# Performance work log

Measured on AMD Instinct MI355X. Metric: run time of the kernel, lower is better.

## Reference

```python
import jax, jax.numpy as jnp
import numpy as np

K, D = 2048, 256
B, H, W = 16, 64, 64
DECAY = 0.99
EPS = 1e-05


def setup_inputs() -> dict:
    key = jax.random.key(0)
    k1, k2, k3 = jax.random.split(key, 3)
    z_e = jax.random.normal(k1, (B, D, H, W), dtype=jnp.float32)
    codebook = jax.random.normal(k2, (K, D), dtype=jnp.float32)
    ema_count = jnp.zeros((K,), dtype=jnp.float32)
    ema_weight = jax.random.normal(k3, (K, D), dtype=jnp.float32)
    return {"z_e": z_e, "codebook": codebook, "ema_count": ema_count, "ema_weight": ema_weight}


def reference(z_e, codebook, ema_count, ema_weight):
    b, d, h, w = z_e.shape
    k = codebook.shape[0]
    # [B, D, H, W] -> [B*H*W, D]
    flat = jnp.transpose(z_e, (0, 2, 3, 1)).reshape(-1, d)
    # squared euclidean distances to each code: [N, K]
    dist = (jnp.sum(flat * flat, axis=1, keepdims=True)
            - 2.0 * (flat @ codebook.T)
            + jnp.sum(codebook * codebook, axis=1))
    idx = jnp.argmin(dist, axis=1)  # [N] int
    # gather nearest codes -> [B, D, H, W]
    z_q = jnp.transpose(codebook[idx].reshape(b, h, w, d), (0, 3, 1, 2))
    # EMA statistics (training path, no_grad in torch)
    n = jax.ops.segment_sum(jnp.ones_like(idx, dtype=flat.dtype), idx, num_segments=k)  # [K]
    dw = jax.ops.segment_sum(flat, idx, num_segments=k)  # [K, D]
    new_ema_count = ema_count * DECAY + (1.0 - DECAY) * n
    new_ema_weight = ema_weight * DECAY + (1.0 - DECAY) * dw
    new_codebook = new_ema_weight / (new_ema_count + EPS)[:, None]
    # commitment loss and straight-through estimator
    loss_commit = jnp.mean(jnp.square(z_e - z_q))
    z_q_st = z_e + jax.lax.stop_gradient(z_q - z_e)
    return (z_q_st, idx.reshape(b, h, w), loss_commit,
            new_codebook, new_ema_count, new_ema_weight)
```

## Files before the change

kernel.cpp:

```cpp
#include <hip/hip_runtime.h>
#include <hip/hip_bf16.h>


#define KC 2048
#define DD 256
#define NB 16
#define HWS 4096
#define NPTS 65536
#define DECAYF 0.99f
#define ONEMD 0.01f
#define EPSF 1e-5f
#define NCH 2
#define MARGIN 0.0625f
#define CHPTS 32
#define FPT 64
#define NLOSS 4096

typedef __attribute__((ext_vector_type(8))) short short8v;
typedef __attribute__((ext_vector_type(16))) float f32x16;

#define WS_IDX     0
#define WS_SORTED  262144
#define WS_CNTI    524288
#define WS_START   532480
#define WS_CURSOR  540672
#define WS_FLAGCNT 548864
#define WS_FLAGS   549120
#define WS_LOSSP   549120
#define WS_CNORM   811264
#define WS_PART    819456
#define WS_CBH     5013760
#define WS_CBL     6062336
#define WS_ZH      7110912
#define WS_ZL      40665344
#define WS_NEED_MFMA 74219776ULL
#define WS_NEED_MID  5013760ULL

#define OUT_ZQ   0
#define OUT_IDX  16777216
#define OUT_LOSS (OUT_IDX + NPTS)
#define OUT_CB   (OUT_LOSS + 1)
#define OUT_CNT  (OUT_CB + KC*DD)
#define OUT_W    (OUT_CNT + KC)

static __device__ __forceinline__ unsigned short f2bf_rn(float x) {
    unsigned u = __builtin_bit_cast(unsigned, x);
    unsigned r = (u + 0x7FFFu + ((u >> 16) & 1u)) >> 16;
    return (unsigned short)r;
}
static __device__ __forceinline__ float bf2f(unsigned short h) {
    unsigned u = ((unsigned)h) << 16;
    return __builtin_bit_cast(float, u);
}
static __device__ __forceinline__ void gload_lds16(const unsigned short* g,
                                                   unsigned short* l) {
    __builtin_amdgcn_global_load_lds(
        (const __attribute__((address_space(1))) void*)g,
        (__attribute__((address_space(3))) void*)l, 16, 0, 0);
}

__global__ __launch_bounds__(256) void prep_kernel(const float* __restrict__ z_e,
                                                   const float* __restrict__ cb,
                                                   float* __restrict__ cnorm,
                                                   unsigned short* __restrict__ cbs_h,
                                                   unsigned short* __restrict__ cbs_l,
                                                   unsigned short* __restrict__ zh,
                                                   unsigned short* __restrict__ zl,
                                                   int* __restrict__ cnti,
                                                   int* __restrict__ flagcnt) {
    const int tid = threadIdx.x;
    if (blockIdx.x >= 4096) {
        int k = (blockIdx.x - 4096) * 256 + tid;
        cnti[k] = 0;
        if (k == 0) *flagcnt = 0;
        const int ct = k >> 5, lc = k & 31;
        const float4* row = reinterpret_cast<const float4*>(cb + (size_t)k * DD);
        float s = 0.f;
        #pragma unroll 4
        for (int chunk = 0; chunk < 32; ++chunk) {
            float4 v0 = row[chunk * 2], v1 = row[chunk * 2 + 1];
            float v[8] = {v0.x, v0.y, v0.z, v0.w, v1.x, v1.y, v1.z, v1.w};
            unsigned short hh[8], ll[8];
            #pragma unroll
            for (int j = 0; j < 8; ++j) {
                s += v[j] * v[j];
                hh[j] = f2bf_rn(v[j]);
                ll[j] = f2bf_rn(v[j] - bf2f(hh[j]));
            }
            const int ks = chunk >> 1, h = chunk & 1;
            size_t dst = (size_t)ct * 8192 + ks * 512 + (h * 32 + lc) * 8;
            *reinterpret_cast<ushort4*>(cbs_h + dst)     = *(ushort4*)&hh[0];
            *reinterpret_cast<ushort4*>(cbs_h + dst + 4) = *(ushort4*)&hh[4];
            *reinterpret_cast<ushort4*>(cbs_l + dst)     = *(ushort4*)&ll[0];
            *reinterpret_cast<ushort4*>(cbs_l + dst + 4) = *(ushort4*)&ll[4];
        }
        cnorm[k] = s;
        return;
    }
    __shared__ float t_lds[64][65];
    const int bid = blockIdx.x;
    const int hw0 = (bid & 63) * 64;
    const int d0 = ((bid >> 6) & 3) * 64;
    const int b = bid >> 8;
    const float* src = z_e + (size_t)b * DD * HWS;
    #pragma unroll
    for (int i = 0; i < 16; ++i) {
        int li = tid + i * 256;
        int d = li >> 6, hw = li & 63;
        t_lds[d][hw] = src[(size_t)(d0 + d) * HWS + hw0 + hw];
    }
    __syncthreads();
    #pragma unroll
    for (int i = 0; i < 16; ++i) {
        int li = tid + i * 256;
        int p = li >> 6, d = li & 63;
        float x = t_lds[d][p];
        unsigned short h = f2bf_rn(x);
        unsigned short l = f2bf_rn(x - bf2f(h));
        size_t o = ((size_t)b * HWS + hw0 + p) * DD + d0 + d;
        zh[o] = h; zl[o] = l;
    }
}

__global__ __launch_bounds__(256) void cnorm_kernel(const float* __restrict__ cb,
                                                    float* __restrict__ cnorm) {
    int k = blockIdx.x * 256 + threadIdx.x;
    if (k < KC) {
        const float4* row = reinterpret_cast<const float4*>(cb + (size_t)k * DD);
        float s = 0.f;
        #pragma unroll 8
        for (int i = 0; i < DD / 4; ++i) {
            float4 v = row[i];
            s += v.x * v.x + v.y * v.y + v.z * v.z + v.w * v.w;
        }
        cnorm[k] = s;
    }
}

__global__ __launch_bounds__(256, 2) void argmin_mfma_kernel(const unsigned short* __restrict__ zh,
                                                             const unsigned short* __restrict__ zl,
                                                             const unsigned short* __restrict__ cbs_h,
                                                             const unsigned short* __restrict__ cbs_l,
                                                             const float* __restrict__ cnorm,
                                                             int* __restrict__ idx_out,
                                                             int* __restrict__ cnti,
                                                             int* __restrict__ flagcnt,
                                                             int* __restrict__ flaglist,
                                                             unsigned long long* __restrict__ fixmin) {
    __shared__ unsigned short lds_cb[2][2][16][512];

    const int tid = threadIdx.x;
    const int w = tid >> 6, lane = tid & 63;
    const int lc = lane & 31, h = lane >> 5;
    const int p = blockIdx.x * 128 + w * 32 + lc;

    const short8v* zhp = reinterpret_cast<const short8v*>(zh + (size_t)p * DD + h * 8);
    const short8v* zlp = reinterpret_cast<const short8v*>(zl + (size_t)p * DD + h * 8);
    short8v bh[16], bl[16];
    #pragma unroll
    for (int ks = 0; ks < 16; ++ks) { bh[ks] = zhp[ks * 2]; bl[ks] = zlp[ks * 2]; }

    auto stage = [&](int ct, int buf) {
        #pragma unroll
        for (int j = 0; j < 8; ++j) {
            const int inst = w * 8 + j;
            const int part = inst >> 4;
            const int ks = inst & 15;
            const unsigned short* src =
                (part ? cbs_l : cbs_h) + (size_t)ct * 8192 + ks * 512 + lane * 8;
            gload_lds16(src, &lds_cb[buf][part][ks][0]);
        }
    };

    float bv1 = 3.4e38f, bv2 = 3.4e38f;
    int bi1 = 0;
    int cur = 0;

    stage(0, 0);
    __syncthreads();

    for (int ct = 0; ct < KC / 32; ++ct) {
        if (ct + 1 < KC / 32) stage(ct + 1, cur ^ 1);

        f32x16 a0, a1, a2;
        #pragma unroll
        for (int i = 0; i < 16; ++i) { a0[i] = 0.f; a1[i] = 0.f; a2[i] = 0.f; }
        #pragma unroll
        for (int ks = 0; ks < 16; ++ks) {
            short8v ah = *reinterpret_cast<const short8v*>(&lds_cb[cur][0][ks][lane * 8]);
            short8v al = *reinterpret_cast<const short8v*>(&lds_cb[cur][1][ks][lane * 8]);
            a0 = __builtin_amdgcn_mfma_f32_32x32x16_bf16(ah, bh[ks], a0, 0, 0, 0);
            a1 = __builtin_amdgcn_mfma_f32_32x32x16_bf16(ah, bl[ks], a1, 0, 0, 0);
            a2 = __builtin_amdgcn_mfma_f32_32x32x16_bf16(al, bh[ks], a2, 0, 0, 0);
        }
        const float* cnb = cnorm + ct * 32 + h * 4;
        #pragma unroll
        for (int g = 0; g < 4; ++g) {
            float4 cn = *reinterpret_cast<const float4*>(cnb + g * 8);
            float cna[4] = {cn.x, cn.y, cn.z, cn.w};
            #pragma unroll
            for (int q = 0; q < 4; ++q) {
                float dot = a0[g * 4 + q] + a1[g * 4 + q] + a2[g * 4 + q];
                float v = fmaf(dot, -2.0f, cna[q]);
                int k = ct * 32 + g * 8 + h * 4 + q;
                bool lt = v < bv1;
                bv2 = fminf(bv2, fmaxf(v, bv1));
                bv1 = fminf(bv1, v);
                bi1 = lt ? k : bi1;
            }
        }
        __syncthreads();
        cur ^= 1;
    }

    float ov1 = __shfl_xor(bv1, 32, 64);
    float ov2 = __shfl_xor(bv2, 32, 64);
    int   oi1 = __shfl_xor(bi1, 32, 64);
    float nv1 = fminf(bv1, ov1);
    float nv2 = fminf(fmaxf(bv1, ov1), fminf(bv2, ov2));
    int ni1 = (ov1 < bv1 || (ov1 == bv1 && oi1 < bi1)) ? oi1 : bi1;

    if (h == 0) {
        idx_out[p] = ni1;
        atomicAdd(&cnti[ni1], 1);
        if (nv2 - nv1 < MARGIN) {
            int pos = atomicAdd(flagcnt, 1);
            flaglist[pos] = p;
            fixmin[pos] = ~0ULL;
        }
    }
}

__global__ __launch_bounds__(256) void fixup_part_kernel(const float* __restrict__ z_e,
                                                         const float* __restrict__ cb,
                                                         const float* __restrict__ cnorm,
                                                         const int* __restrict__ flagcnt,
                                                         const int* __restrict__ flaglist,
                                                         unsigned long long* __restrict__ fixmin) {
    __shared__ float As[64][FPT + 4];
    __shared__ float Bs[64][64 + 4];
    __shared__ float rv[FPT][16];
    __shared__ int   ri[FPT][16];
    __shared__ int   zo[FPT];

    const int tid = threadIdx.x;
    const int tx = tid & 15, ty = tid >> 4;
    const int tot = *flagcnt;
    const int base = blockIdx.x * FPT;
    if (base >= tot) return;
    const int cnt = min(FPT, tot - base);
    const int kt = blockIdx.y * 64;

    if (tid < FPT) {
        int n = flaglist[base + ((tid < cnt) ? tid : 0)];
        zo[tid] = (n >> 12) * DD * HWS + (n & 4095);
    }
    __syncthreads();

    float acc[4][4] = {};
    for (int dc = 0; dc < DD; dc += 64) {
        #pragma unroll
        for (int i = 0; i < 16; ++i) {
            int li = tid + i * 256;
            int d = li >> 6, pp = li & 63;
            As[d][pp] = z_e[(size_t)zo[pp] + (size_t)(dc + d) * HWS];
        }
        #pragma unroll
        for (int i = 0; i < 16; ++i) {
            int li = tid + i * 256;
            int k = li >> 6, d = li & 63;
            Bs[d][k] = cb[(size_t)(kt + k) * DD + dc + d];
        }
        __syncthreads();
        #pragma unroll
        for (int d = 0; d < 64; ++d) {
            const float4 a4 = *reinterpret_cast<const float4*>(&As[d][ty * 4]);
            const float4 b4 = *reinterpret_cast<const float4*>(&Bs[d][tx * 4]);
            const float a[4] = {a4.x, a4.y, a4.z, a4.w};
            const float bb[4] = {b4.x, b4.y, b4.z, b4.w};
            #pragma unroll
            for (int j = 0; j < 4; ++j)
                #pragma unroll
                for (int i = 0; i < 4; ++i)
                    acc[j][i] = fmaf(a[j], bb[i], acc[j][i]);
        }
        __syncthreads();
    }

    float bestv[4]; int besti[4];
    #pragma unroll
    for (int j = 0; j < 4; ++j) { bestv[j] = 3.4e38f; besti[j] = 0; }
    #pragma unroll
    for (int i = 0; i < 4; ++i) {
        int k = kt + tx * 4 + i;
        float c = cnorm[k];
        #pragma unroll
        for (int j = 0; j < 4; ++j) {
            float dist = c - 2.0f * acc[j][i];
            if (dist < bestv[j]) { bestv[j] = dist; besti[j] = k; }
        }
    }
    #pragma unroll
    for (int j = 0; j < 4; ++j) { rv[ty * 4 + j][tx] = bestv[j]; ri[ty * 4 + j][tx] = besti[j]; }
    __syncthreads();

    if (tid < cnt) {
        float bv = rv[tid][0]; int bi = ri[tid][0];
        #pragma unroll
        for (int t = 1; t < 16; ++t) {
            float v = rv[tid][t]; int i2 = ri[tid][t];
            if (v < bv || (v == bv && i2 < bi)) { bv = v; bi = i2; }
        }
        unsigned uv = __float_as_uint(bv);
        uv = (uv & 0x80000000u) ? ~uv : (uv | 0x80000000u);
        unsigned long long key = ((unsigned long long)uv << 32) | (unsigned)bi;
        atomicMin(&fixmin[base + tid], key);
    }
}

__global__ __launch_bounds__(256) void fixup_apply_kernel(const int* __restrict__ flagcnt,
                                                          const int* __restrict__ flaglist,
                                                          const unsigned long long* __restrict__ fixmin,
                                                          int* __restrict__ idx_out,
                                                          int* __restrict__ cnti) {
    int f = blockIdx.x * 256 + threadIdx.x;
    if (f < *flagcnt) {
        int n = flaglist[f];
        int nk = (int)(fixmin[f] & 0xFFFFFFFFull);
        int ok = idx_out[n];
        if (nk != ok) {
            atomicSub(&cnti[ok], 1);
            atomicAdd(&cnti[nk], 1);
            idx_out[n] = nk;
        }
    }
}

#define PT 64
#define KT 64
#define DC 64
__global__ __launch_bounds__(256) void argmin_kernel(const float* __restrict__ z_e,
                                                     const float* __restrict__ cb,
                                                     const float* __restrict__ cnorm,
                                                     int* __restrict__ idx_out) {
    __shared__ float As[DC][PT + 4];
    __shared__ float Bs[DC][KT + 4];
    __shared__ float rv[PT][16];
    __shared__ int   ri[PT][16];
    const int tid = threadIdx.x;
    const int tx = tid & 15, ty = tid >> 4;
    const int n0 = blockIdx.x * PT;
    const int b = n0 >> 12;
    const int hw0 = n0 & 4095;
    const float* zb = z_e + (size_t)b * DD * HWS + hw0;
    float bestv[4]; int besti[4];
    #pragma unroll
    for (int j = 0; j < 4; ++j) { bestv[j] = 3.4e38f; besti[j] = 0; }
    for (int kt = 0; kt < KC; kt += KT) {
        float acc[4][4] = {};
        for (int dc = 0; dc < DD; dc += DC) {
            #pragma unroll
            for (int i = 0; i < 16; ++i) {
                int li = tid + i * 256;
                int d = li >> 6, pp = li & 63;
                As[d][pp] = zb[(size_t)(dc + d) * HWS + pp];
            }
            #pragma unroll
            for (int i = 0; i < 16; ++i) {
                int li = tid + i * 256;
                int k = li >> 6, d = li & 63;
                Bs[d][k] = cb[(size_t)(kt + k) * DD + dc + d];
            }
            __syncthreads();
            #pragma unroll
            for (int d = 0; d < DC; ++d) {
                const float4 a4 = *reinterpret_cast<const float4*>(&As[d][ty * 4]);
                const float4 b4 = *reinterpret_cast<const float4*>(&Bs[d][tx * 4]);
                const float a[4] = {a4.x, a4.y, a4.z, a4.w};
                const float bb[4] = {b4.x, b4.y, b4.z, b4.w};
                #pragma unroll
                for (int j = 0; j < 4; ++j)
                    #pragma unroll
                    for (int i = 0; i < 4; ++i)
                        acc[j][i] = fmaf(a[j], bb[i], acc[j][i]);
            }
            __syncthreads();
        }
        #pragma unroll
        for (int i = 0; i < 4; ++i) {
            int k = kt + tx * 4 + i;
            float c = cnorm[k];
            #pragma unroll
            for (int j = 0; j < 4; ++j) {
                float dist = c - 2.0f * acc[j][i];
                if (dist < bestv[j]) { bestv[j] = dist; besti[j] = k; }
            }
        }
    }
    #pragma unroll
    for (int j = 0; j < 4; ++j) { rv[ty * 4 + j][tx] = bestv[j]; ri[ty * 4 + j][tx] = besti[j]; }
    __syncthreads();
    if (tid < PT) {
        float bv = rv[tid][0]; int bi = ri[tid][0];
        #pragma unroll
        for (int t = 1; t < 16; ++t) {
            float v = rv[tid][t]; int i2 = ri[tid][t];
            if (v < bv || (v == bv && i2 < bi)) { bv = v; bi = i2; }
        }
        idx_out[n0 + tid] = bi;
    }
}

__global__ __launch_bounds__(256) void hist_kernel(const int* __restrict__ idx,
                                                   int* __restrict__ cnti) {
    int n = blockIdx.x * 256 + threadIdx.x;
    atomicAdd(&cnti[idx[n]], 1);
}

__global__ __launch_bounds__(256) void scan_kernel(const int* __restrict__ cnt,
                                                   int* __restrict__ start,
                                                   int* __restrict__ cursor) {
    __shared__ int ps[256];
    const int t = threadIdx.x;
    int v[8], s = 0;
    #pragma unroll
    for (int j = 0; j < 8; ++j) { v[j] = cnt[t * 8 + j]; s += v[j]; }
    ps[t] = s;
    __syncthreads();
    for (int off = 1; off < 256; off <<= 1) {
        int x = (t >= off) ? ps[t - off] : 0;
        __syncthreads();
        ps[t] += x;
        __syncthreads();
    }
    int base = ps[t] - s;
    #pragma unroll
    for (int j = 0; j < 8; ++j) { start[t * 8 + j] = base; cursor[t * 8 + j] = base; base += v[j]; }
}

__global__ __launch_bounds__(256) void scatter_ids_kernel(const int* __restrict__ idx,
                                                          int* __restrict__ cursor,
                                                          int* __restrict__ sorted,
                                                          float* __restrict__ out_idxf,
                                                          float* __restrict__ dwacc) {
    int n = blockIdx.x * 256 + threadIdx.x;
    int k = idx[n];
    out_idxf[n] = (float)k;
    int pos = atomicAdd(&cursor[k], 1);
    sorted[pos] = n;
    #pragma unroll
    for (int i = 0; i < (KC * DD) / NPTS; ++i)
        dwacc[n + i * NPTS] = 0.f;
}

__global__ __launch_bounds__(256) void dw_chunk_kernel(const unsigned short* __restrict__ zh,
                                                       const unsigned short* __restrict__ zl,
                                                       const int* __restrict__ sorted,
                                                       const int* __restrict__ idx,
                                                       float* __restrict__ dwacc) {
    const int t = threadIdx.x;
    const int base = blockIdx.x * CHPTS;
    int kcur = idx[sorted[base]];
    float acc = 0.f;
    for (int i = 0; i < CHPTS; ++i) {
        const int n = sorted[base + i];
        const int k = idx[n];
        if (k != kcur) {
            atomicAdd(&dwacc[(size_t)kcur * DD + t], acc);
            acc = 0.f; kcur = k;
        }
        acc += bf2f(zh[(size_t)n * DD + t]) + bf2f(zl[(size_t)n * DD + t]);
    }
    atomicAdd(&dwacc[(size_t)kcur * DD + t], acc);
}

__global__ __launch_bounds__(256) void dw_direct_kernel(const float* __restrict__ z_e,
                                                        const int* __restrict__ sorted,
                                                        const int* __restrict__ start,
                                                        const int* __restrict__ cnti,
                                                        float* __restrict__ part) {
    const int k = blockIdx.x, c = blockIdx.y, t = threadIdx.x;
    const int s0 = start[k], cnt = cnti[k];
    float acc = 0.f;
    for (int p = c; p < cnt; p += NCH) {
        int n = sorted[s0 + p];
        int b = n >> 12, hw = n & 4095;
        acc += z_e[(size_t)b * DD * HWS + (size_t)t * HWS + hw];
    }
    part[((size_t)k * NCH + c) * DD + t] = acc;
}

__global__ __launch_bounds__(256) void zq_loss_kernel(const float* __restrict__ z_e,
                                                      const float* __restrict__ cb,
                                                      const int* __restrict__ idx,
                                                      float* __restrict__ out_zq,
                                                      float* __restrict__ lossp) {
    const int tid = threadIdx.x;
    const size_t base = ((size_t)blockIdx.x * 256 + tid) * 16;
    const int hw = (int)(base & 4095);
    const int d = (int)((base >> 12) & 255);
    const int b = (int)(base >> 20);
    const int n0 = b * HWS + hw;

    const int4* ip = reinterpret_cast<const int4*>(idx + n0);
    const float4* zp = reinterpret_cast<const float4*>(z_e + base);
    float4* op = reinterpret_cast<float4*>(out_zq + base);

    float ls = 0.f;
    #pragma unroll
    for (int g = 0; g < 4; ++g) {
        int4 i4 = ip[g];
        float4 z4 = zp[g];
        int kk[4] = {i4.x, i4.y, i4.z, i4.w};
        float zz[4] = {z4.x, z4.y, z4.z, z4.w};
        float o4[4];
        #pragma unroll
        for (int q = 0; q < 4; ++q) {
            float qv = cb[(size_t)kk[q] * DD + d];
            o4[q] = zz[q] + (qv - zz[q]);
            float df = zz[q] - qv;
            ls += df * df;
        }
        float4 w4; w4.x = o4[0]; w4.y = o4[1]; w4.z = o4[2]; w4.w = o4[3];
        op[g] = w4;
    }

    #pragma unroll
    for (int off = 32; off > 0; off >>= 1) ls += __shfl_down(ls, off, 64);
    __shared__ float wsum[4];
    if ((tid & 63) == 0) wsum[tid >> 6] = ls;
    __syncthreads();
    if (tid == 0) lossp[blockIdx.x] = wsum[0] + wsum[1] + wsum[2] + wsum[3];
}

__global__ __launch_bounds__(256) void finalize_dw_kernel(const float* __restrict__ ema_count,
                                                          const float* __restrict__ ema_weight,
                                                          const int* __restrict__ cnti,
                                                          const float* __restrict__ dwacc,
                                                          const float* __restrict__ lossp,
                                                          float* __restrict__ out_cb,
                                                          float* __restrict__ out_cnt,
                                                          float* __restrict__ out_w,
                                                          float* __restrict__ out_loss) {
    const int t = blockIdx.x * 256 + threadIdx.x;
    const int k = t >> 8, d = t & 255;
    const float nc = ema_count[k] * DECAYF + ONEMD * (float)cnti[k];
    const float nw = ema_weight[t] * DECAYF + ONEMD * dwacc[t];
    out_w[t] = nw;
    out_cb[t] = nw / (nc + EPSF);
    if (d == 0) out_cnt[k] = nc;

    if (blockIdx.x == 0) {
        __shared__ double sd[256];
        const int tid = threadIdx.x;
        double s = 0.0;
        for (int i = tid; i < NLOSS; i += 256) s += (double)lossp[i];
        sd[tid] = s;
        __syncthreads();
        for (int off = 128; off > 0; off >>= 1) {
            if (tid < off) sd[tid] += sd[tid + off];
            __syncthreads();
        }
        if (tid == 0) out_loss[0] = (float)(sd[0] / 16777216.0);
    }
}

__global__ __launch_bounds__(256) void finalize_part_kernel(const float* __restrict__ ema_count,
                                                            const float* __restrict__ ema_weight,
                                                            const int* __restrict__ cnti,
                                                            const float* __restrict__ part,
                                                            const float* __restrict__ lossp,
                                                            float* __restrict__ out_cb,
                                                            float* __restrict__ out_cnt,
                                                            float* __restrict__ out_w,
                                                            float* __restrict__ out_loss) {
    const int t = blockIdx.x * 256 + threadIdx.x;
    const int k = t >> 8, d = t & 255;
    float dw = 0.f;
    #pragma unroll
    for (int c = 0; c < NCH; ++c) dw += part[((size_t)k * NCH + c) * DD + d];
    const float nc = ema_count[k] * DECAYF + ONEMD * (float)cnti[k];
    const float nw = ema_weight[t] * DECAYF + ONEMD * dw;
    out_w[t] = nw;
    out_cb[t] = nw / (nc + EPSF);
    if (d == 0) out_cnt[k] = nc;

    if (blockIdx.x == 0) {
        __shared__ double sd[256];
        const int tid = threadIdx.x;
        double s = 0.0;
        for (int i = tid; i < NLOSS; i += 256) s += (double)lossp[i];
        sd[tid] = s;
        __syncthreads();
        for (int off = 128; off > 0; off >>= 1) {
            if (tid < off) sd[tid] += sd[tid + off];
            __syncthreads();
        }
        if (tid == 0) out_loss[0] = (float)(sd[0] / 16777216.0);
    }
}

extern "C" void kernel_launch(void* const* d_in, const int* in_sizes, int n_in,
                              void* d_out, int out_size, void* d_ws, size_t ws_size,
                              hipStream_t stream) {
    const float* z_e       = (const float*)d_in[0];
    const float* codebook  = (const float*)d_in[1];
    const float* ema_count = (const float*)d_in[2];
    const float* ema_weight= (const float*)d_in[3];
    float* out = (float*)d_out;
    char* ws = (char*)d_ws;

    int*   ws_idx    = (int*)(ws + WS_IDX);
    int*   ws_sorted = (int*)(ws + WS_SORTED);
    int*   ws_cnti   = (int*)(ws + WS_CNTI);
    int*   ws_start  = (int*)(ws + WS_START);
    int*   ws_cursor = (int*)(ws + WS_CURSOR);
    int*   ws_flagc  = (int*)(ws + WS_FLAGCNT);
    int*   ws_flags  = (int*)(ws + WS_FLAGS);
    float* ws_lossp  = (float*)(ws + WS_LOSSP);
    float* ws_cnorm  = (float*)(ws + WS_CNORM);
    unsigned long long* ws_fixmin = (unsigned long long*)(ws + WS_PART);
    float* ws_dwacc  = (float*)(ws + WS_PART);
    float* ws_part   = (float*)(ws + WS_PART);
    unsigned short* ws_cbh = (unsigned short*)(ws + WS_CBH);
    unsigned short* ws_cbl = (unsigned short*)(ws + WS_CBL);
    unsigned short* ws_zh  = (unsigned short*)(ws + WS_ZH);
    unsigned short* ws_zl  = (unsigned short*)(ws + WS_ZL);

    const bool mfma_path = (ws_size >= WS_NEED_MFMA);
    const bool mid_path  = (ws_size >= WS_NEED_MID);

    if (mfma_path) {
        prep_kernel<<<4104, 256, 0, stream>>>(z_e, codebook, ws_cnorm, ws_cbh, ws_cbl,
                                              ws_zh, ws_zl, ws_cnti, ws_flagc);
        argmin_mfma_kernel<<<NPTS / 128, 256, 0, stream>>>(ws_zh, ws_zl, ws_cbh, ws_cbl,
                                                           ws_cnorm, ws_idx, ws_cnti,
                                                           ws_flagc, ws_flags, ws_fixmin);
        fixup_part_kernel<<<dim3(NPTS / FPT, KC / 64), 256, 0, stream>>>(z_e, codebook, ws_cnorm,
                                                                         ws_flagc, ws_flags,
                                                                         ws_fixmin);
        fixup_apply_kernel<<<NPTS / 256, 256, 0, stream>>>(ws_flagc, ws_flags, ws_fixmin,
                                                           ws_idx, ws_cnti);
        zq_loss_kernel<<<NLOSS, 256, 0, stream>>>(z_e, codebook, ws_idx,
                                                  out + OUT_ZQ, ws_lossp);
        scan_kernel<<<1, 256, 0, stream>>>(ws_cnti, ws_start, ws_cursor);
        scatter_ids_kernel<<<NPTS / 256, 256, 0, stream>>>(ws_idx, ws_cursor, ws_sorted,
                                                           out + OUT_IDX, ws_dwacc);
        dw_chunk_kernel<<<NPTS / CHPTS, 256, 0, stream>>>(ws_zh, ws_zl, ws_sorted,
                                                          ws_idx, ws_dwacc);
        finalize_dw_kernel<<<(KC * DD) / 256, 256, 0, stream>>>(ema_count, ema_weight,
                                                                ws_cnti, ws_dwacc, ws_lossp,
                                                                out + OUT_CB, out + OUT_CNT,
                                                                out + OUT_W, out + OUT_LOSS);
    } else if (mid_path) {
        hipMemsetAsync(ws + WS_CNTI, 0, (size_t)(WS_FLAGCNT + 256 - WS_CNTI), stream);
        cnorm_kernel<<<(KC + 255) / 256, 256, 0, stream>>>(codebook, ws_cnorm);
        argmin_kernel<<<NPTS / PT, 256, 0, stream>>>(z_e, codebook, ws_cnorm, ws_idx);
        zq_loss_kernel<<<NLOSS, 256, 0, stream>>>(z_e, codebook, ws_idx,
                                                  out + OUT_ZQ, ws_lossp);
        hist_kernel<<<NPTS / 256, 256, 0, stream>>>(ws_idx, ws_cnti);
        scan_kernel<<<1, 256, 0, stream>>>(ws_cnti, ws_start, ws_cursor);
        scatter_ids_kernel<<<NPTS / 256, 256, 0, stream>>>(ws_idx, ws_cursor, ws_sorted,
                                                           out + OUT_IDX, ws_part);
        dw_direct_kernel<<<dim3(KC, NCH), 256, 0, stream>>>(z_e, ws_sorted,
                                                            ws_start, ws_cnti, ws_part + KC * DD);
        finalize_part_kernel<<<(KC * DD) / 256, 256, 0, stream>>>(ema_count, ema_weight,
                                                                  ws_cnti, ws_part + KC * DD,
                                                                  ws_lossp,
                                                                  out + OUT_CB, out + OUT_CNT,
                                                                  out + OUT_W, out + OUT_LOSS);
    }
}
```

Baseline: 409.3 us.

## Fuse fixup-apply with scan, fold scatter into zq kernel, grid-stride fixup

```diff
diff --git a/kernel.cpp b/kernel.cpp
--- a/kernel.cpp
+++ b/kernel.cpp
@@ -246,85 +246,90 @@
     const int tid = threadIdx.x;
     const int tx = tid & 15, ty = tid >> 4;
     const int tot = *flagcnt;
-    const int base = blockIdx.x * FPT;
-    if (base >= tot) return;
-    const int cnt = min(FPT, tot - base);
     const int kt = blockIdx.y * 64;
 
-    if (tid < FPT) {
-        int n = flaglist[base + ((tid < cnt) ? tid : 0)];
-        zo[tid] = (n >> 12) * DD * HWS + (n & 4095);
-    }
-    __syncthreads();
-
-    float acc[4][4] = {};
-    for (int dc = 0; dc < DD; dc += 64) {
-        #pragma unroll
-        for (int i = 0; i < 16; ++i) {
-            int li = tid + i * 256;
-            int d = li >> 6, pp = li & 63;
-            As[d][pp] = z_e[(size_t)zo[pp] + (size_t)(dc + d) * HWS];
-        }
-        #pragma unroll
-        for (int i = 0; i < 16; ++i) {
-            int li = tid + i * 256;
-            int k = li >> 6, d = li & 63;
-            Bs[d][k] = cb[(size_t)(kt + k) * DD + dc + d];
-        }
-        __syncthreads();
-        #pragma unroll
-        for (int d = 0; d < 64; ++d) {
-            const float4 a4 = *reinterpret_cast<const float4*>(&As[d][ty * 4]);
-            const float4 b4 = *reinterpret_cast<const float4*>(&Bs[d][tx * 4]);
-            const float a[4] = {a4.x, a4.y, a4.z, a4.w};
-            const float bb[4] = {b4.x, b4.y, b4.z, b4.w};
-            #pragma unroll
-            for (int j = 0; j < 4; ++j)
+    for (int cbk = blockIdx.x; cbk * FPT < tot; cbk += gridDim.x) {
+        const int base = cbk * FPT;
+        const int cnt = min(FPT, tot - base);
+        __syncthreads();
+        if (tid < FPT) {
+            int n = flaglist[base + ((tid < cnt) ? tid : 0)];
+            zo[tid] = (n >> 12) * DD * HWS + (n & 4095);
+        }
+        __syncthreads();
+
+        float acc[4][4] = {};
+        for (int dc = 0; dc < DD; dc += 64) {
+            #pragma unroll
+            for (int i = 0; i < 16; ++i) {
+                int li = tid + i * 256;
+                int d = li >> 6, pp = li & 63;
+                As[d][pp] = z_e[(size_t)zo[pp] + (size_t)(dc + d) * HWS];
+            }
+            #pragma unroll
+            for (int i = 0; i < 16; ++i) {
+                int li = tid + i * 256;
+                int k = li >> 6, d = li & 63;
+                Bs[d][k] = cb[(size_t)(kt + k) * DD + dc + d];
+            }
+            __syncthreads();
+            #pragma unroll
+            for (int d = 0; d < 64; ++d) {
+                const float4 a4 = *reinterpret_cast<const float4*>(&As[d][ty * 4]);
+                const float4 b4 = *reinterpret_cast<const float4*>(&Bs[d][tx * 4]);
+                const float a[4] = {a4.x, a4.y, a4.z, a4.w};
+                const float bb[4] = {b4.x, b4.y, b4.z, b4.w};
                 #pragma unroll
-                for (int i = 0; i < 4; ++i)
-                    acc[j][i] = fmaf(a[j], bb[i], acc[j][i]);
-        }
-        __syncthreads();
-    }
-
-    float bestv[4]; int besti[4];
-    #pragma unroll
-    for (int j = 0; j < 4; ++j) { bestv[j] = 3.4e38f; besti[j] = 0; }
-    #pragma unroll
-    for (int i = 0; i < 4; ++i) {
-        int k = kt + tx * 4 + i;
-        float c = cnorm[k];
-        #pragma unroll
-        for (int j = 0; j < 4; ++j) {
-            float dist = c - 2.0f * acc[j][i];
-            if (dist < bestv[j]) { bestv[j] = dist; besti[j] = k; }
-        }
-    }
-    #pragma unroll
-    for (int j = 0; j < 4; ++j) { rv[ty * 4 + j][tx] = bestv[j]; ri[ty * 4 + j][tx] = besti[j]; }
-    __syncthreads();
-
-    if (tid < cnt) {
-        float bv = rv[tid][0]; int bi = ri[tid][0];
-        #pragma unroll
-        for (int t = 1; t < 16; ++t) {
-            float v = rv[tid][t]; int i2 = ri[tid][t];
-            if (v < bv || (v == bv && i2 < bi)) { bv = v; bi = i2; }
-        }
-        unsigned uv = __float_as_uint(bv);
-        uv = (uv & 0x80000000u) ? ~uv : (uv | 0x80000000u);
-        unsigned long long key = ((unsigned long long)uv << 32) | (unsigned)bi;
-        atomicMin(&fixmin[base + tid], key);
-    }
-}
-
-__global__ __launch_bounds__(256) void fixup_apply_kernel(const int* __restrict__ flagcnt,
-                                                          const int* __restrict__ flaglist,
-                                                          const unsigned long long* __restrict__ fixmin,
-                                                          int* __restrict__ idx_out,
-                                                          int* __restrict__ cnti) {
-    int f = blockIdx.x * 256 + threadIdx.x;
-    if (f < *flagcnt) {
+                for (int j = 0; j < 4; ++j)
+                    #pragma unroll
+                    for (int i = 0; i < 4; ++i)
+                        acc[j][i] = fmaf(a[j], bb[i], acc[j][i]);
+            }
+            __syncthreads();
+        }
+
+        float bestv[4]; int besti[4];
+        #pragma unroll
+        for (int j = 0; j < 4; ++j) { bestv[j] = 3.4e38f; besti[j] = 0; }
+        #pragma unroll
+        for (int i = 0; i < 4; ++i) {
+            int k = kt + tx * 4 + i;
+            float c = cnorm[k];
+            #pragma unroll
+            for (int j = 0; j < 4; ++j) {
+                float dist = c - 2.0f * acc[j][i];
+                if (dist < bestv[j]) { bestv[j] = dist; besti[j] = k; }
+            }
+        }
+        #pragma unroll
+        for (int j = 0; j < 4; ++j) { rv[ty * 4 + j][tx] = bestv[j]; ri[ty * 4 + j][tx] = besti[j]; }
+        __syncthreads();
+
+        if (tid < cnt) {
+            float bv = rv[tid][0]; int bi = ri[tid][0];
+            #pragma unroll
+            for (int t = 1; t < 16; ++t) {
+                float v = rv[tid][t]; int i2 = ri[tid][t];
+                if (v < bv || (v == bv && i2 < bi)) { bv = v; bi = i2; }
+            }
+            unsigned uv = __float_as_uint(bv);
+            uv = (uv & 0x80000000u) ? ~uv : (uv | 0x80000000u);
+            unsigned long long key = ((unsigned long long)uv << 32) | (unsigned)bi;
+            atomicMin(&fixmin[base + tid], key);
+        }
+    }
+}
+
+__global__ __launch_bounds__(256) void scan_apply_kernel(const int* __restrict__ flagcnt,
+                                                         const int* __restrict__ flaglist,
+                                                         const unsigned long long* __restrict__ fixmin,
+                                                         int* __restrict__ idx_out,
+                                                         int* __restrict__ cnti,
+                                                         int* __restrict__ start,
+                                                         int* __restrict__ cursor) {
+    const int t = threadIdx.x;
+    const int tot = *flagcnt;
+    for (int f = t; f < tot; f += 256) {
         int n = flaglist[f];
         int nk = (int)(fixmin[f] & 0xFFFFFFFFull);
         int ok = idx_out[n];
@@ -334,6 +339,23 @@
             idx_out[n] = nk;
         }
     }
+    __syncthreads();
+
+    __shared__ int ps[256];
+    int v[8], s = 0;
+    #pragma unroll
+    for (int j = 0; j < 8; ++j) { v[j] = cnti[t * 8 + j]; s += v[j]; }
+    ps[t] = s;
+    __syncthreads();
+    for (int off = 1; off < 256; off <<= 1) {
+        int x = (t >= off) ? ps[t - off] : 0;
+        __syncthreads();
+        ps[t] += x;
+        __syncthreads();
+    }
+    int base = ps[t] - s;
+    #pragma unroll
+    for (int j = 0; j < 8; ++j) { start[t * 8 + j] = base; cursor[t * 8 + j] = base; base += v[j]; }
 }
 
 #define PT 64
@@ -417,40 +439,15 @@
     atomicAdd(&cnti[idx[n]], 1);
 }
 
-__global__ __launch_bounds__(256) void scan_kernel(const int* __restrict__ cnt,
-                                                   int* __restrict__ start,
-                                                   int* __restrict__ cursor) {
-    __shared__ int ps[256];
-    const int t = threadIdx.x;
-    int v[8], s = 0;
-    #pragma unroll
-    for (int j = 0; j < 8; ++j) { v[j] = cnt[t * 8 + j]; s += v[j]; }
-    ps[t] = s;
-    __syncthreads();
-    for (int off = 1; off < 256; off <<= 1) {
-        int x = (t >= off) ? ps[t - off] : 0;
-        __syncthreads();
-        ps[t] += x;
-        __syncthreads();
-    }
-    int base = ps[t] - s;
-    #pragma unroll
-    for (int j = 0; j < 8; ++j) { start[t * 8 + j] = base; cursor[t * 8 + j] = base; base += v[j]; }
-}
-
 __global__ __launch_bounds__(256) void scatter_ids_kernel(const int* __restrict__ idx,
                                                           int* __restrict__ cursor,
                                                           int* __restrict__ sorted,
-                                                          float* __restrict__ out_idxf,
-                                                          float* __restrict__ dwacc) {
+                                                          float* __restrict__ out_idxf) {
     int n = blockIdx.x * 256 + threadIdx.x;
     int k = idx[n];
     out_idxf[n] = (float)k;
     int pos = atomicAdd(&cursor[k], 1);
     sorted[pos] = n;
-    #pragma unroll
-    for (int i = 0; i < (KC * DD) / NPTS; ++i)
-        dwacc[n + i * NPTS] = 0.f;
 }
 
 __global__ __launch_bounds__(256) void dw_chunk_kernel(const unsigned short* __restrict__ zh,
@@ -490,11 +487,16 @@
     part[((size_t)k * NCH + c) * DD + t] = acc;
 }
 
-__global__ __launch_bounds__(256) void zq_loss_kernel(const float* __restrict__ z_e,
-                                                      const float* __restrict__ cb,
-                                                      const int* __restrict__ idx,
-                                                      float* __restrict__ out_zq,
-                                                      float* __restrict__ lossp) {
+__global__ __launch_bounds__(256) void zq_scatter_kernel(const float* __restrict__ z_e,
+                                                         const float* __restrict__ cb,
+                                                         const int* __restrict__ idx,
+                                                         float* __restrict__ out_zq,
+                                                         float* __restrict__ lossp,
+                                                         int* __restrict__ cursor,
+                                                         int* __restrict__ sorted,
+                                                         float* __restrict__ out_idxf,
+                                                         float* __restrict__ dwacc,
+                                                         int fuse_tail) {
     const int tid = threadIdx.x;
     const size_t base = ((size_t)blockIdx.x * 256 + tid) * 16;
     const int hw = (int)(base & 4095);
@@ -531,6 +533,17 @@
     if ((tid & 63) == 0) wsum[tid >> 6] = ls;
     __syncthreads();
     if (tid == 0) lossp[blockIdx.x] = wsum[0] + wsum[1] + wsum[2] + wsum[3];
+
+    if (fuse_tail && blockIdx.x < 256) {
+        int n = blockIdx.x * 256 + tid;
+        int k = idx[n];
+        out_idxf[n] = (float)k;
+        int pos = atomicAdd(&cursor[k], 1);
+        sorted[pos] = n;
+        #pragma unroll
+        for (int i = 0; i < (KC * DD) / NPTS; ++i)
+            dwacc[n + i * NPTS] = 0.f;
+    }
 }
 
 __global__ __launch_bounds__(256) void finalize_dw_kernel(const float* __restrict__ ema_count,
@@ -636,16 +649,15 @@
         argmin_mfma_kernel<<<NPTS / 128, 256, 0, stream>>>(ws_zh, ws_zl, ws_cbh, ws_cbl,
                                                            ws_cnorm, ws_idx, ws_cnti,
                                                            ws_flagc, ws_flags, ws_fixmin);
-        fixup_part_kernel<<<dim3(NPTS / FPT, KC / 64), 256, 0, stream>>>(z_e, codebook, ws_cnorm,
-                                                                         ws_flagc, ws_flags,
-                                                                         ws_fixmin);
-        fixup_apply_kernel<<<NPTS / 256, 256, 0, stream>>>(ws_flagc, ws_flags, ws_fixmin,
-                                                           ws_idx, ws_cnti);
-        zq_loss_kernel<<<NLOSS, 256, 0, stream>>>(z_e, codebook, ws_idx,
-                                                  out + OUT_ZQ, ws_lossp);
-        scan_kernel<<<1, 256, 0, stream>>>(ws_cnti, ws_start, ws_cursor);
-        scatter_ids_kernel<<<NPTS / 256, 256, 0, stream>>>(ws_idx, ws_cursor, ws_sorted,
-                                                           out + OUT_IDX, ws_dwacc);
+        fixup_part_kernel<<<dim3(128, KC / 64), 256, 0, stream>>>(z_e, codebook, ws_cnorm,
+                                                                  ws_flagc, ws_flags,
+                                                                  ws_fixmin);
+        scan_apply_kernel<<<1, 256, 0, stream>>>(ws_flagc, ws_flags, ws_fixmin,
+                                                 ws_idx, ws_cnti, ws_start, ws_cursor);
+        zq_scatter_kernel<<<NLOSS, 256, 0, stream>>>(z_e, codebook, ws_idx,
+                                                     out + OUT_ZQ, ws_lossp,
+                                                     ws_cursor, ws_sorted,
+                                                     out + OUT_IDX, ws_dwacc, 1);
         dw_chunk_kernel<<<NPTS / CHPTS, 256, 0, stream>>>(ws_zh, ws_zl, ws_sorted,
                                                           ws_idx, ws_dwacc);
         finalize_dw_kernel<<<(KC * DD) / 256, 256, 0, stream>>>(ema_count, ema_weight,
@@ -656,12 +668,15 @@
         hipMemsetAsync(ws + WS_CNTI, 0, (size_t)(WS_FLAGCNT + 256 - WS_CNTI), stream);
         cnorm_kernel<<<(KC + 255) / 256, 256, 0, stream>>>(codebook, ws_cnorm);
         argmin_kernel<<<NPTS / PT, 256, 0, stream>>>(z_e, codebook, ws_cnorm, ws_idx);
-        zq_loss_kernel<<<NLOSS, 256, 0, stream>>>(z_e, codebook, ws_idx,
-                                                  out + OUT_ZQ, ws_lossp);
         hist_kernel<<<NPTS / 256, 256, 0, stream>>>(ws_idx, ws_cnti);
-        scan_kernel<<<1, 256, 0, stream>>>(ws_cnti, ws_start, ws_cursor);
+        scan_apply_kernel<<<1, 256, 0, stream>>>(ws_flagc, ws_flags, ws_fixmin,
+                                                 ws_idx, ws_cnti, ws_start, ws_cursor);
+        zq_scatter_kernel<<<NLOSS, 256, 0, stream>>>(z_e, codebook, ws_idx,
+                                                     out + OUT_ZQ, ws_lossp,
+                                                     ws_cursor, ws_sorted,
+                                                     out + OUT_IDX, ws_part, 0);
         scatter_ids_kernel<<<NPTS / 256, 256, 0, stream>>>(ws_idx, ws_cursor, ws_sorted,
-                                                           out + OUT_IDX, ws_part);
+                                                           out + OUT_IDX);
         dw_direct_kernel<<<dim3(KC, NCH), 256, 0, stream>>>(z_e, ws_sorted,
                                                             ws_start, ws_cnti, ws_part + KC * DD);
         finalize_part_kernel<<<(KC * DD) / 256, 256, 0, stream>>>(ema_count, ema_weight,
```

Measured after the change: 403.5 us (median of 2 runs). About the same (-1.4%).
